# Performance work log

Hardware: AMD Instinct MI355X
Metric: run time of the kernel (lower is better)

Reference implementation:

```python
import jax, jax.numpy as jnp
import numpy as np

N = 100_000   # nodes
C = 32        # classes
E = 3_200_000 # edges


def setup_inputs() -> dict:
    key = jax.random.key(0)
    k1, k2, k3, k4, k5 = jax.random.split(key, 5)
    edge_index = jax.random.randint(k1, (2, E), 0, N, dtype=jnp.int32)
    edge_weight = jax.random.uniform(k2, (E,), dtype=jnp.float32) + 0.1  # positive weights
    inputs = jax.random.normal(k3, (N, C), dtype=jnp.float32)
    labels = jax.random.randint(k4, (N,), 0, C)
    y = jax.nn.one_hot(labels, C, dtype=jnp.float32)  # torch.where(y[:, i]) implies one-hot labels
    sample_mask = jax.random.bernoulli(k5, 0.5, (N,))
    return {"edge_index": edge_index, "edge_weight": edge_weight,
            "inputs": inputs, "y": y, "sample_mask": sample_mask}


def _normalize_sparse(edge_index, edge_weight, n):
    # normalize_sparse_tensor: add self-loops (weight 1), then D^{-1/2} A D^{-1/2}
    loop = jnp.arange(n, dtype=edge_index.dtype)
    row = jnp.concatenate([edge_index[0], loop])
    col = jnp.concatenate([edge_index[1], loop])
    w = jnp.concatenate([edge_weight, jnp.ones((n,), edge_weight.dtype)])
    deg = jax.ops.segment_sum(w, row, num_segments=n)
    dinv = jnp.where(deg > 0, jax.lax.rsqrt(deg), 0.0)
    vals = dinv[row] * w * dinv[col]
    return row, col, vals


def reference(edge_index, edge_weight, inputs, y, sample_mask):
    n, c = inputs.shape
    row, col, vals = _normalize_sparse(edge_index, edge_weight, n)

    p = jax.nn.softmax(inputs, axis=1)
    m = sample_mask.astype(p.dtype)[:, None]
    p = p * (1.0 - m) + y * m          # replace predictions by labels on masked nodes
    ym = y * m                          # labels only on masked nodes

    # nodeH = raw_normed_adj @ p   (sparse spmm)  -> (n, c)
    nodeH = jax.ops.segment_sum(vals[:, None] * p[col], row, num_segments=n)

    # per-class mean of nodeH over nodes with label i (one-hot => sum/count)
    cnt = ym.sum(axis=0)                         # (c,)
    H = (ym.T @ nodeH) / cnt[:, None]            # (c, c); NaN rows if class empty

    # NaN fixups (identity when no NaNs present)
    Hn = jnp.isnan(H)
    H = jnp.where(Hn, H.T, H)
    Hn = jnp.isnan(H)
    H0 = jnp.where(Hn, jnp.zeros_like(H), H)
    miss = (1.0 - H0.sum(axis=1, keepdims=True)) / Hn.sum(axis=1, keepdims=True).astype(H.dtype)
    H = jnp.where(Hn, miss, H0)

    # makeDoubleStochasticH: iterate col-norm then row-norm; 'delta' = ||H||_1 (as in source)
    def cond(state):
        _, i, d = state
        return (d >= 1e-12) & (i < 3000)

    def body(state):
        Hc, i, _ = state
        Hc = Hc / Hc.sum(axis=0, keepdims=True)
        Hc = Hc / Hc.sum(axis=1, keepdims=True)
        return Hc, i + 1, jnp.abs(Hc).sum()

    H, _, _ = jax.lax.while_loop(cond, body, (H, jnp.int32(0), jnp.float32(1e30)))
    return H
```

## Files before the change

### kernel.cpp

```cpp
#include <hip/hip_runtime.h>
#include <hip/hip_fp16.h>


#define RS 32768
#define RSH 15
#define BDEG 64
#define W 200
#define NBKTMAX 512
#define BCAP 2304
#define LCAP 2048
#define NSC 512
#define NPR NBKTMAX
#define NTOT (1 + NPR + NSC)
#define NRED 16
#define RPER ((NTOT + NRED - 1) / NRED)
#define PPAD 204
#define BVW 3200

__global__ __launch_bounds__(1024) void
k_deg(const int* __restrict__ ei, const float* __restrict__ ew,
      __half* __restrict__ slab, const unsigned char* __restrict__ mask_bytes,
      int* __restrict__ flag, float* __restrict__ Hg, float* __restrict__ cnt,
      int* __restrict__ gCnt, int E_, int R) {
  __shared__ float h[RS];
  if (blockIdx.x == 0) {
    Hg[threadIdx.x] = 0.f;
    if (threadIdx.x < 32) cnt[threadIdx.x] = 0.f;
    if (threadIdx.x < NBKTMAX) gCnt[threadIdx.x] = 0;
    __shared__ int shi;
    if (threadIdx.x == 0) shi = 0;
    __syncthreads();
    int acc = mask_bytes[threadIdx.x * 4 + 1] | mask_bytes[threadIdx.x * 4 + 2]
            | mask_bytes[threadIdx.x * 4 + 3];
    if (acc) atomicOr(&shi, 1);
    __syncthreads();
    if (threadIdx.x == 0) *flag = (shi != 0) ? 1 : 0;
  }
  int r = blockIdx.x % R;
  int sl = blockIdx.x / R;
  for (int i = threadIdx.x; i < RS; i += 1024) h[i] = 0.f;
  __syncthreads();
  int lo = r << RSH;
  int Q = E_ >> 2;
  int q0 = (int)((long long)Q * sl / BDEG);
  int q1 = (int)((long long)Q * (sl + 1) / BDEG);
  const int4* ei4 = (const int4*)ei;
  const float4* ew4 = (const float4*)ew;
  int q = q0 + threadIdx.x;
  for (; q + 1024 < q1; q += 2048) {
    int4 ia = ei4[q], ib = ei4[q + 1024];
    float4 wa = ew4[q], wb = ew4[q + 1024];
    unsigned o0 = (unsigned)(ia.x - lo), o1 = (unsigned)(ia.y - lo);
    unsigned o2 = (unsigned)(ia.z - lo), o3 = (unsigned)(ia.w - lo);
    unsigned o4 = (unsigned)(ib.x - lo), o5 = (unsigned)(ib.y - lo);
    unsigned o6 = (unsigned)(ib.z - lo), o7 = (unsigned)(ib.w - lo);
    if (o0 < RS) atomicAdd(&h[o0], wa.x);
    if (o1 < RS) atomicAdd(&h[o1], wa.y);
    if (o2 < RS) atomicAdd(&h[o2], wa.z);
    if (o3 < RS) atomicAdd(&h[o3], wa.w);
    if (o4 < RS) atomicAdd(&h[o4], wb.x);
    if (o5 < RS) atomicAdd(&h[o5], wb.y);
    if (o6 < RS) atomicAdd(&h[o6], wb.z);
    if (o7 < RS) atomicAdd(&h[o7], wb.w);
  }
  for (; q < q1; q += 1024) {
    int4 idx = ei4[q];
    float4 w = ew4[q];
    unsigned o0 = (unsigned)(idx.x - lo), o1 = (unsigned)(idx.y - lo);
    unsigned o2 = (unsigned)(idx.z - lo), o3 = (unsigned)(idx.w - lo);
    if (o0 < RS) atomicAdd(&h[o0], w.x);
    if (o1 < RS) atomicAdd(&h[o1], w.y);
    if (o2 < RS) atomicAdd(&h[o2], w.z);
    if (o3 < RS) atomicAdd(&h[o3], w.w);
  }
  if (sl == BDEG - 1) {
    for (int e = (Q << 2) + threadIdx.x; e < E_; e += 1024) {
      unsigned off = (unsigned)(ei[e] - lo);
      if (off < RS) atomicAdd(&h[off], ew[e]);
    }
  }
  __syncthreads();
  __half* dst = slab + ((size_t)r * BDEG + sl) * RS;
  for (int i = threadIdx.x; i < RS; i += 1024) dst[i] = __float2half(h[i]);
}

__global__ void k_node(const float* __restrict__ x, const float* __restrict__ y,
                       const void* __restrict__ maskp, const int* __restrict__ flag,
                       const __half* __restrict__ slab, int2* __restrict__ ninfo,
                       __half* __restrict__ p16, float* __restrict__ Hg,
                       float* __restrict__ cnt, unsigned* __restrict__ bitvec, int Nn) {
  __shared__ float scnt[32], sdiag[32];
  if (threadIdx.x < 32) { scnt[threadIdx.x] = 0.f; sdiag[threadIdx.x] = 0.f; }
  __syncthreads();
  int n = blockIdx.x * blockDim.x + threadIdx.x;
  bool inb = (n < Nn);
  bool byteMask = (*flag != 0);
  bool msk = false;
  if (inb)
    msk = byteMask ? (((const unsigned char*)maskp)[n] != 0)
                   : (((const int*)maskp)[n] != 0);
  unsigned long long bm = __ballot(msk);
  if ((threadIdx.x & 63) == 0)
    ((unsigned long long*)bitvec)[n >> 6] = bm;
  if (inb) {
    const __half* sl = slab + ((size_t)(n >> RSH) * BDEG) * RS + (n & (RS - 1));
    float d = 0.f;
    #pragma unroll 8
    for (int bb = 0; bb < BDEG; ++bb) d += __half2float(sl[(size_t)bb * RS]);
    float dinv = rsqrtf(d + 1.0f);
    int a = -1;
    if (msk) {
      const float4* yi = (const float4*)(y + (size_t)n * 32);
      #pragma unroll
      for (int q = 0; q < 8; ++q) {
        float4 v = yi[q];
        if (v.x == 1.f) a = q * 4 + 0;
        if (v.y == 1.f) a = q * 4 + 1;
        if (v.z == 1.f) a = q * 4 + 2;
        if (v.w == 1.f) a = q * 4 + 3;
      }
      atomicAdd(&scnt[a], 1.f);
      atomicAdd(&sdiag[a], dinv * dinv);
    } else {
      const float4* xi = (const float4*)(x + (size_t)n * 32);
      float xs[32];
      #pragma unroll
      for (int q = 0; q < 8; ++q) {
        float4 v = xi[q];
        xs[q*4+0] = v.x; xs[q*4+1] = v.y; xs[q*4+2] = v.z; xs[q*4+3] = v.w;
      }
      float mx = -3.4e38f;
      #pragma unroll
      for (int i = 0; i < 32; ++i) mx = fmaxf(mx, xs[i]);
      float s = 0.f;
      #pragma unroll
      for (int i = 0; i < 32; ++i) { xs[i] = __expf(xs[i] - mx); s += xs[i]; }
      float inv = 1.f / s;
      union { short sh[32]; int4 v[4]; } u;
      #pragma unroll
      for (int i = 0; i < 32; ++i)
        u.sh[i] = __half_as_short(__float2half(xs[i] * inv));
      int4* po = (int4*)(p16 + (size_t)n * 32);
      #pragma unroll
      for (int q = 0; q < 4; ++q) po[q] = u.v[q];
    }
    int2 ni; ni.x = __float_as_int(dinv); ni.y = a;
    ninfo[n] = ni;
  }
  __syncthreads();
  if (threadIdx.x < 32) {
    if (scnt[threadIdx.x] != 0.f) atomicAdd(&cnt[threadIdx.x], scnt[threadIdx.x]);
    if (sdiag[threadIdx.x] != 0.f) atomicAdd(&Hg[threadIdx.x * 33], sdiag[threadIdx.x]);
  }
}

__global__ __launch_bounds__(1024) void
k_bucket(const int* __restrict__ ei, const float* __restrict__ ew,
         const int2* __restrict__ ninfo, const unsigned* __restrict__ bitvec,
         int2* __restrict__ gBucket, int* __restrict__ gCnt,
         float* __restrict__ scatSlab, int E_) {
  __shared__ float sH[1024];
  __shared__ int2 list[LCAP];
  __shared__ int lcnt;
  __shared__ int bcnt[NBKTMAX];
  __shared__ int gbase[NBKTMAX];
  __shared__ int bplace[NBKTMAX];
  __shared__ unsigned sbv[BVW];
  sH[threadIdx.x] = 0.f;
  if (threadIdx.x == 0) lcnt = 0;
  if (threadIdx.x < NBKTMAX) { bcnt[threadIdx.x] = 0; bplace[threadIdx.x] = 0; }
  for (int i = threadIdx.x; i < BVW; i += 1024) sbv[i] = bitvec[i];
  __syncthreads();
  int E4 = E_ >> 2;
  int q0 = (int)((long long)E4 * blockIdx.x / NSC);
  int q1 = (int)((long long)E4 * (blockIdx.x + 1) / NSC);
  for (int q = q0 + threadIdx.x; q < q1; q += 1024) {
    int4 rr = ((const int4*)ei)[q];
    int4 cc = ((const int4*)(ei + E_))[q];
    float4 ww = ((const float4*)ew)[q];
    int rs[4] = {rr.x, rr.y, rr.z, rr.w};
    int cs[4] = {cc.x, cc.y, cc.z, cc.w};
    float wv[4] = {ww.x, ww.y, ww.z, ww.w};
    bool act[4];
    #pragma unroll
    for (int k = 0; k < 4; ++k)
      act[k] = (sbv[(unsigned)rs[k] >> 5] >> (rs[k] & 31)) & 1;
    int2 nr[4], nc[4];
    #pragma unroll
    for (int k = 0; k < 4; ++k)
      if (act[k]) { nr[k] = ninfo[rs[k]]; nc[k] = ninfo[cs[k]]; }
    #pragma unroll
    for (int k = 0; k < 4; ++k) {
      if (act[k]) {
        float val = __int_as_float(nr[k].x) * wv[k] * __int_as_float(nc[k].x);
        if (nc[k].y >= 0) {
          atomicAdd(&sH[nr[k].y * 32 + nc[k].y], val);
        } else {
          int pos = atomicAdd(&lcnt, 1);
          if (pos < LCAP) list[pos] = make_int2((cs[k] << 5) | nr[k].y, __float_as_int(val));
        }
      }
    }
  }
  if (blockIdx.x == NSC - 1) {
    for (int e = (E4 << 2) + threadIdx.x; e < E_; e += 1024) {
      int r = ei[e];
      if (!((sbv[(unsigned)r >> 5] >> (r & 31)) & 1)) continue;
      int2 nr = ninfo[r];
      int c = ei[E_ + e];
      int2 nc = ninfo[c];
      float val = __int_as_float(nr.x) * ew[e] * __int_as_float(nc.x);
      if (nc.y >= 0) {
        atomicAdd(&sH[nr.y * 32 + nc.y], val);
      } else {
        int pos = atomicAdd(&lcnt, 1);
        if (pos < LCAP) list[pos] = make_int2((c << 5) | nr.y, __float_as_int(val));
      }
    }
  }
  __syncthreads();
  int nl = min(lcnt, LCAP);
  for (int i = threadIdx.x; i < nl; i += 1024)
    atomicAdd(&bcnt[(list[i].x >> 5) / W], 1);
  __syncthreads();
  if (threadIdx.x < NBKTMAX) {
    int n = bcnt[threadIdx.x];
    gbase[threadIdx.x] = (n > 0) ? atomicAdd(&gCnt[threadIdx.x], n) : 0;
  }
  __syncthreads();
  for (int i = threadIdx.x; i < nl; i += 1024) {
    int2 rec = list[i];
    int bkt = (rec.x >> 5) / W;
    int slot = atomicAdd(&bplace[bkt], 1);
    int dst = gbase[bkt] + slot;
    if (dst < BCAP) gBucket[(size_t)bkt * BCAP + dst] = rec;
  }
  __syncthreads();
  scatSlab[(size_t)blockIdx.x * 1024 + threadIdx.x] = sH[threadIdx.x];
}

__global__ __launch_bounds__(1024) void
k_process(const int2* __restrict__ gBucket, const int* __restrict__ gCnt,
          const __half* __restrict__ p16, float* __restrict__ procSlab, int Nn) {
  __shared__ float TlocT[32 * W];
  __shared__ __half plocT[32 * PPAD];
  int k = blockIdx.x;
  int c0 = k * W;
  int Wb = min(c0 + W, Nn) - c0;
  for (int i = threadIdx.x; i < 32 * W; i += 1024) TlocT[i] = 0.f;
  __syncthreads();
  if (Wb > 0) {
    for (int i = threadIdx.x; i < Wb * 32; i += 1024) {
      int c = i >> 5, b = i & 31;
      plocT[b * PPAD + c] = p16[(size_t)(c0 + c) * 32 + b];
    }
    int n = min(gCnt[k], BCAP);
    const int2* bk = gBucket + (size_t)k * BCAP;
    for (int i = threadIdx.x; i < n; i += 1024) {
      int2 rec = bk[i];
      atomicAdd(&TlocT[(rec.x & 31) * W + ((rec.x >> 5) - c0)], __int_as_float(rec.y));
    }
  }
  __syncthreads();
  int a = threadIdx.x >> 5;
  int b = threadIdx.x & 31;
  float acc0 = 0.f, acc1 = 0.f, acc2 = 0.f, acc3 = 0.f;
  int c = 0;
  for (; c + 3 < Wb; c += 4) {
    float4 tv = *(const float4*)&TlocT[a * W + c];
    short4 ps = *(const short4*)&plocT[b * PPAD + c];
    acc0 += tv.x * __half2float(__short_as_half(ps.x));
    acc1 += tv.y * __half2float(__short_as_half(ps.y));
    acc2 += tv.z * __half2float(__short_as_half(ps.z));
    acc3 += tv.w * __half2float(__short_as_half(ps.w));
  }
  for (; c < Wb; ++c)
    acc0 += TlocT[a * W + c] * __half2float(plocT[b * PPAD + c]);
  procSlab[(size_t)k * 1024 + threadIdx.x] = (acc0 + acc1) + (acc2 + acc3);
}

__global__ __launch_bounds__(1024) void
k_red(const float* __restrict__ allSlabs, float* __restrict__ red) {
  int k0 = blockIdx.x * RPER;
  int k1 = min(k0 + RPER, NTOT);
  float s = 0.f;
  for (int k = k0; k < k1; ++k) s += allSlabs[(size_t)k * 1024 + threadIdx.x];
  red[(size_t)blockIdx.x * 1024 + threadIdx.x] = s;
}

__global__ __launch_bounds__(1024) void
k_sinkhorn(const float* __restrict__ red, const float* __restrict__ cnt,
           float* __restrict__ out) {
  __shared__ float sHH[1024];
  int t = threadIdx.x;
  float s = 0.f;
  #pragma unroll
  for (int k = 0; k < NRED; ++k) s += red[(size_t)k * 1024 + t];
  sHH[t] = s;
  __syncthreads();
  int j = t;
  if (j >= 32) return;
  float cj = cnt[j];
  float Hcol[32], Hrow[32];
  #pragma unroll
  for (int i = 0; i < 32; ++i) Hcol[i] = sHH[i * 32 + j];
  #pragma unroll
  for (int i = 0; i < 32; ++i) Hcol[i] /= __shfl(cj, i);
  #pragma unroll
  for (int k = 0; k < 32; ++k) Hrow[k] = sHH[j * 32 + k] / cj;
  float u = 1.f, v = 1.f;
  for (int it = 0; it < 40; ++it) {
    float a0 = 0.f, a1 = 0.f, a2 = 0.f, a3 = 0.f;
    #pragma unroll
    for (int i = 0; i < 32; i += 4) {
      a0 += Hcol[i+0] * __shfl(u, i+0);
      a1 += Hcol[i+1] * __shfl(u, i+1);
      a2 += Hcol[i+2] * __shfl(u, i+2);
      a3 += Hcol[i+3] * __shfl(u, i+3);
    }
    v = 1.f / ((a0 + a1) + (a2 + a3));
    a0 = a1 = a2 = a3 = 0.f;
    #pragma unroll
    for (int k = 0; k < 32; k += 4) {
      a0 += Hrow[k+0] * __shfl(v, k+0);
      a1 += Hrow[k+1] * __shfl(v, k+1);
      a2 += Hrow[k+2] * __shfl(v, k+2);
      a3 += Hrow[k+3] * __shfl(v, k+3);
    }
    u = 1.f / ((a0 + a1) + (a2 + a3));
  }
  #pragma unroll
  for (int i = 0; i < 32; ++i) out[i * 32 + j] = __shfl(u, i) * Hcol[i] * v;
}

extern "C" void kernel_launch(void* const* d_in, const int* in_sizes, int n_in,
                              void* d_out, int out_size, void* d_ws, size_t ws_size,
                              hipStream_t stream) {
  const int*   ei   = (const int*)d_in[0];
  const float* ew   = (const float*)d_in[1];
  const float* x    = (const float*)d_in[2];
  const float* y    = (const float*)d_in[3];
  const void*  mask = d_in[4];
  float* out = (float*)d_out;
  int E_ = in_sizes[1];
  int Nn = in_sizes[2] / 32;
  int R = (Nn + RS - 1) >> RSH;

  char* ws = (char*)d_ws;
  size_t o = 0;
  float* cnt = (float*)(ws + o);    o += 128;
  int*   flag = (int*)(ws + o);     o += 128;
  int*   gCnt = (int*)(ws + o);     o += NBKTMAX * 4;
  float* allSlabs = (float*)(ws + o);
  float* Hg       = allSlabs;
  float* procSlab = allSlabs + 1024;
  float* scatSlab = allSlabs + (size_t)(1 + NPR) * 1024;
  o += (size_t)NTOT * 4096;
  float* red = (float*)(ws + o);    o += (size_t)NRED * 4096;
  int2*  gBucket = (int2*)(ws + o); o += (size_t)NBKTMAX * BCAP * 8;
  __half* slab = (__half*)(ws + o); o += (size_t)R * BDEG * RS * 2;
  int2*  ninfo = (int2*)(ws + o);   o += (size_t)Nn * 8;
  __half* p16 = (__half*)(ws + o);  o += (size_t)Nn * 64;
  unsigned* gbv = (unsigned*)(ws + o); o += (size_t)BVW * 4;

  int nb = (Nn + 255) / 256;
  k_deg<<<R * BDEG, 1024, 0, stream>>>(ei, ew, slab, (const unsigned char*)mask,
                                       flag, Hg, cnt, gCnt, E_, R);
  k_node<<<nb, 256, 0, stream>>>(x, y, mask, flag, slab, ninfo, p16, Hg, cnt, gbv, Nn);
  k_bucket<<<NSC, 1024, 0, stream>>>(ei, ew, ninfo, gbv, gBucket, gCnt, scatSlab, E_);
  k_process<<<NPR, 1024, 0, stream>>>(gBucket, gCnt, p16, procSlab, Nn);
  k_red<<<NRED, 1024, 0, stream>>>(allSlabs, red);
  k_sinkhorn<<<1, 1024, 0, stream>>>(red, cnt, out);
}
```

Baseline: 225.1 us.

## Defer column-side normalization and label scatter from bucketing to per-bucket processing

The bucketing kernel no longer gathers ninfo for the column node. It sends every active edge to its column bucket, carrying only row-side dinv times the weight. The process kernel loads dinv and label for its column range into shared memory. It then either accumulates into a local 32x32 H tile for labelled columns or into the dense T matrix for the rest. This removes one random global gather per edge and the scatter slab reduction, at the cost of doubling bucket capacities, more bucket traffic, and more atomics in k_process.

```diff
diff --git a/kernel.cpp b/kernel.cpp
--- a/kernel.cpp
+++ b/kernel.cpp
@@ -7,11 +7,11 @@
 #define BDEG 64
 #define W 200
 #define NBKTMAX 512
-#define BCAP 2304
-#define LCAP 2048
+#define BCAP 4608
+#define LCAP 4096
 #define NSC 512
 #define NPR NBKTMAX
-#define NTOT (1 + NPR + NSC)
+#define NTOT (1 + NPR)
 #define NRED 16
 #define RPER ((NTOT + NRED - 1) / NRED)
 #define PPAD 204
@@ -157,16 +157,13 @@
 __global__ __launch_bounds__(1024) void
 k_bucket(const int* __restrict__ ei, const float* __restrict__ ew,
          const int2* __restrict__ ninfo, const unsigned* __restrict__ bitvec,
-         int2* __restrict__ gBucket, int* __restrict__ gCnt,
-         float* __restrict__ scatSlab, int E_) {
-  __shared__ float sH[1024];
+         int2* __restrict__ gBucket, int* __restrict__ gCnt, int E_) {
   __shared__ int2 list[LCAP];
   __shared__ int lcnt;
   __shared__ int bcnt[NBKTMAX];
   __shared__ int gbase[NBKTMAX];
   __shared__ int bplace[NBKTMAX];
   __shared__ unsigned sbv[BVW];
-  sH[threadIdx.x] = 0.f;
   if (threadIdx.x == 0) lcnt = 0;
   if (threadIdx.x < NBKTMAX) { bcnt[threadIdx.x] = 0; bplace[threadIdx.x] = 0; }
   for (int i = threadIdx.x; i < BVW; i += 1024) sbv[i] = bitvec[i];
@@ -185,20 +182,16 @@
     #pragma unroll
     for (int k = 0; k < 4; ++k)
       act[k] = (sbv[(unsigned)rs[k] >> 5] >> (rs[k] & 31)) & 1;
-    int2 nr[4], nc[4];
+    int2 nr[4];
     #pragma unroll
     for (int k = 0; k < 4; ++k)
-      if (act[k]) { nr[k] = ninfo[rs[k]]; nc[k] = ninfo[cs[k]]; }
+      if (act[k]) nr[k] = ninfo[rs[k]];
     #pragma unroll
     for (int k = 0; k < 4; ++k) {
       if (act[k]) {
-        float val = __int_as_float(nr[k].x) * wv[k] * __int_as_float(nc[k].x);
-        if (nc[k].y >= 0) {
-          atomicAdd(&sH[nr[k].y * 32 + nc[k].y], val);
-        } else {
-          int pos = atomicAdd(&lcnt, 1);
-          if (pos < LCAP) list[pos] = make_int2((cs[k] << 5) | nr[k].y, __float_as_int(val));
-        }
+        float val = __int_as_float(nr[k].x) * wv[k];
+        int pos = atomicAdd(&lcnt, 1);
+        if (pos < LCAP) list[pos] = make_int2((cs[k] << 5) | nr[k].y, __float_as_int(val));
       }
     }
   }
@@ -208,14 +201,9 @@
       if (!((sbv[(unsigned)r >> 5] >> (r & 31)) & 1)) continue;
       int2 nr = ninfo[r];
       int c = ei[E_ + e];
-      int2 nc = ninfo[c];
-      float val = __int_as_float(nr.x) * ew[e] * __int_as_float(nc.x);
-      if (nc.y >= 0) {
-        atomicAdd(&sH[nr.y * 32 + nc.y], val);
-      } else {
-        int pos = atomicAdd(&lcnt, 1);
-        if (pos < LCAP) list[pos] = make_int2((c << 5) | nr.y, __float_as_int(val));
-      }
+      float val = __int_as_float(nr.x) * ew[e];
+      int pos = atomicAdd(&lcnt, 1);
+      if (pos < LCAP) list[pos] = make_int2((c << 5) | nr.y, __float_as_int(val));
     }
   }
   __syncthreads();
@@ -235,19 +223,27 @@
     int dst = gbase[bkt] + slot;
     if (dst < BCAP) gBucket[(size_t)bkt * BCAP + dst] = rec;
   }
-  __syncthreads();
-  scatSlab[(size_t)blockIdx.x * 1024 + threadIdx.x] = sH[threadIdx.x];
 }
 
 __global__ __launch_bounds__(1024) void
 k_process(const int2* __restrict__ gBucket, const int* __restrict__ gCnt,
-          const __half* __restrict__ p16, float* __restrict__ procSlab, int Nn) {
+          const int2* __restrict__ ninfo, const __half* __restrict__ p16,
+          float* __restrict__ procSlab, int Nn) {
   __shared__ float TlocT[32 * W];
   __shared__ __half plocT[32 * PPAD];
+  __shared__ float H32[1024];
+  __shared__ float ldin[W];
+  __shared__ int   llab[W];
   int k = blockIdx.x;
   int c0 = k * W;
   int Wb = min(c0 + W, Nn) - c0;
   for (int i = threadIdx.x; i < 32 * W; i += 1024) TlocT[i] = 0.f;
+  H32[threadIdx.x] = 0.f;
+  if ((int)threadIdx.x < Wb) {
+    int2 ni = ninfo[c0 + threadIdx.x];
+    ldin[threadIdx.x] = __int_as_float(ni.x);
+    llab[threadIdx.x] = ni.y;
+  }
   __syncthreads();
   if (Wb > 0) {
     for (int i = threadIdx.x; i < Wb * 32; i += 1024) {
@@ -258,7 +254,12 @@
     const int2* bk = gBucket + (size_t)k * BCAP;
     for (int i = threadIdx.x; i < n; i += 1024) {
       int2 rec = bk[i];
-      atomicAdd(&TlocT[(rec.x & 31) * W + ((rec.x >> 5) - c0)], __int_as_float(rec.y));
+      int cl = (rec.x >> 5) - c0;
+      int a = rec.x & 31;
+      float v = __int_as_float(rec.y) * ldin[cl];
+      int b = llab[cl];
+      if (b >= 0) atomicAdd(&H32[a * 32 + b], v);
+      else        atomicAdd(&TlocT[a * W + cl], v);
     }
   }
   __syncthreads();
@@ -276,7 +277,8 @@
   }
   for (; c < Wb; ++c)
     acc0 += TlocT[a * W + c] * __half2float(plocT[b * PPAD + c]);
-  procSlab[(size_t)k * 1024 + threadIdx.x] = (acc0 + acc1) + (acc2 + acc3);
+  procSlab[(size_t)k * 1024 + threadIdx.x] =
+      (acc0 + acc1) + (acc2 + acc3) + H32[threadIdx.x];
 }
 
 __global__ __launch_bounds__(1024) void
@@ -354,7 +356,6 @@
   float* allSlabs = (float*)(ws + o);
   float* Hg       = allSlabs;
   float* procSlab = allSlabs + 1024;
-  float* scatSlab = allSlabs + (size_t)(1 + NPR) * 1024;
   o += (size_t)NTOT * 4096;
   float* red = (float*)(ws + o);    o += (size_t)NRED * 4096;
   int2*  gBucket = (int2*)(ws + o); o += (size_t)NBKTMAX * BCAP * 8;
@@ -367,8 +368,8 @@
   k_deg<<<R * BDEG, 1024, 0, stream>>>(ei, ew, slab, (const unsigned char*)mask,
                                        flag, Hg, cnt, gCnt, E_, R);
   k_node<<<nb, 256, 0, stream>>>(x, y, mask, flag, slab, ninfo, p16, Hg, cnt, gbv, Nn);
-  k_bucket<<<NSC, 1024, 0, stream>>>(ei, ew, ninfo, gbv, gBucket, gCnt, scatSlab, E_);
-  k_process<<<NPR, 1024, 0, stream>>>(gBucket, gCnt, p16, procSlab, Nn);
+  k_bucket<<<NSC, 1024, 0, stream>>>(ei, ew, ninfo, gbv, gBucket, gCnt, E_);
+  k_process<<<NPR, 1024, 0, stream>>>(gBucket, gCnt, ninfo, p16, procSlab, Nn);
   k_red<<<NRED, 1024, 0, stream>>>(allSlabs, red);
   k_sinkhorn<<<1, 1024, 0, stream>>>(red, cnt, out);
 }
```

Result: faster. 219.1 us (-2.7%).
